# Performance work log

Measured on AMD Instinct MI355X. Metric: run time of the kernel, lower is better.

## Reference

```python
import jax, jax.numpy as jnp
import numpy as np

DIM = 1024
EXP = 4           # expansion_factor
NUM_EXPERTS = 4
BATCH, SEQ = 4, 4096


def setup_inputs() -> dict:
    key = jax.random.key(0)
    ks = jax.random.split(key, 6)
    x = jax.random.normal(ks[0], (BATCH, SEQ, DIM), dtype=jnp.float32)
    token_mask = jax.random.randint(ks[1], (BATCH, SEQ), 0, NUM_EXPERTS, dtype=jnp.int32)
    hid = DIM * EXP
    s1 = 1.0 / np.sqrt(DIM)
    s2 = 1.0 / np.sqrt(hid)
    # nn.Linear layout: weight [out_features, in_features]
    w1 = jax.random.uniform(ks[2], (hid, DIM), minval=-s1, maxval=s1, dtype=jnp.float32)
    b1 = jax.random.uniform(ks[3], (hid,), minval=-s1, maxval=s1, dtype=jnp.float32)
    w2 = jax.random.uniform(ks[4], (DIM, hid), minval=-s2, maxval=s2, dtype=jnp.float32)
    b2 = jax.random.uniform(ks[5], (DIM,), minval=-s2, maxval=s2, dtype=jnp.float32)
    return {"x": x, "w1": w1, "b1": b1, "w2": w2, "b2": b2, "token_mask": token_mask}


def _nested_ffn(x, w1, b1, w2, b2, token_mask):
    dim = x.shape[-1]            # in_features of proj1
    out_dim = w2.shape[0]        # out_features of proj2 (== dim)
    # Expert m uses the first D_m = width >> (E-1-m) features (matryoshka nesting).
    # Expand (proj1): truncating input features to D_m and doing a full GEMM is
    # exactly equivalent to zeroing features >= D_m, so we mask then do one GEMM.
    d_in = dim >> (NUM_EXPERTS - 1 - token_mask)             # [B,S]
    in_mask = jnp.arange(dim) < d_in[..., None]              # [B,S,dim]
    h = jnp.einsum('bsd,fd->bsf', jnp.where(in_mask, x, jnp.zeros((), x.dtype)), w1) + b1
    h = jax.nn.gelu(h, approximate=False)                    # torch nn.GELU() default = erf
    # Contract (proj2): expert m produces only the first D_m outputs (incl. bias),
    # padded with zeros -> compute full GEMM then mask outputs.
    d_out = out_dim >> (NUM_EXPERTS - 1 - token_mask)        # [B,S]
    out_mask = jnp.arange(out_dim) < d_out[..., None]        # [B,S,out_dim]
    y = jnp.einsum('bsf,df->bsd', h, w2) + b2
    return jnp.where(out_mask, y, jnp.zeros((), y.dtype))


def reference(x, w1, b1, w2, b2, token_mask):
    return _nested_ffn(x, w1, b1, w2, b2, token_mask)
```

## Files before the change

kernel.cpp:

```cpp
#include <hip/hip_runtime.h>
#include <hip/hip_bf16.h>


typedef __bf16 bf16x8 __attribute__((ext_vector_type(8)));
typedef float f32x4 __attribute__((ext_vector_type(4)));

#define M_TOK   16384
#define DIM     1024
#define HID     4096

#define META_T     31
#define META_BLK   64
#define META_MAP   256
#define META_RT    2560

__device__ inline unsigned int pk_bf16(float a, float b) {
  unsigned int r;
  asm("v_cvt_pk_bf16_f32 %0, %1, %2" : "=v"(r) : "v"(a), "v"(b));
  return r;
}

__device__ inline float gelu_f(float v) {
  float v2 = v * v;
  float w = v * fmaf(0.10294324f, v2, 2.30220830f);
  float e = __builtin_amdgcn_exp2f(-w);
  return v * __builtin_amdgcn_rcpf(1.0f + e);
}

__device__ inline void async_copy16(const void* g, void* s) {
  __builtin_amdgcn_global_load_lds(
      (const __attribute__((address_space(1))) unsigned int*)g,
      (__attribute__((address_space(3))) unsigned int*)s,
      16, 0, 0);
}

template<int ROWS, int LDK>
__device__ inline void stage_tile(const unsigned short* __restrict__ g,
                                  int row0, int k0, char* lds) {
  const char* gbase = (const char*)g;
  int tid = threadIdx.x;
#pragma unroll
  for (int i = 0; i < ROWS / 32; ++i) {
    int q = i * 256 + tid;
    int r = q >> 3;
    int c = q & 7;
    int gc = c ^ (r & 7);
    const void* gp = gbase + ((size_t)(row0 + r) * LDK + (size_t)k0 + gc * 8) * 2;
    async_copy16(gp, lds + (size_t)q * 16);
  }
}

__global__ __launch_bounds__(1024) void sort_kernel(const int* __restrict__ tm,
                                                    int* __restrict__ meta) {
  __shared__ int cnt[1024][5];
  __shared__ int sbase[5];
  __shared__ int cb[128];
  __shared__ int pfx[129];
  int tid = threadIdx.x;

  int c0 = 0, c1 = 0, c2 = 0, c3 = 0;
  unsigned int epack = 0;
  int4 tv[4];
#pragma unroll
  for (int j = 0; j < 4; ++j)
    tv[j] = *(const int4*)(tm + tid * 16 + j * 4);
#pragma unroll
  for (int j = 0; j < 4; ++j) {
    int e;
    e = tv[j].x; epack |= (unsigned)e << (2 * (4 * j + 0)); c0 += (e == 0); c1 += (e == 1); c2 += (e == 2); c3 += (e == 3);
    e = tv[j].y; epack |= (unsigned)e << (2 * (4 * j + 1)); c0 += (e == 0); c1 += (e == 1); c2 += (e == 2); c3 += (e == 3);
    e = tv[j].z; epack |= (unsigned)e << (2 * (4 * j + 2)); c0 += (e == 0); c1 += (e == 1); c2 += (e == 2); c3 += (e == 3);
    e = tv[j].w; epack |= (unsigned)e << (2 * (4 * j + 3)); c0 += (e == 0); c1 += (e == 1); c2 += (e == 2); c3 += (e == 3);
  }
  cnt[tid][0] = c0; cnt[tid][1] = c1; cnt[tid][2] = c2; cnt[tid][3] = c3;
  __syncthreads();
  for (int s = 1; s < 1024; s <<= 1) {
    int v0 = 0, v1 = 0, v2 = 0, v3 = 0;
    if (tid >= s) {
      v0 = cnt[tid - s][0]; v1 = cnt[tid - s][1];
      v2 = cnt[tid - s][2]; v3 = cnt[tid - s][3];
    }
    __syncthreads();
    cnt[tid][0] += v0; cnt[tid][1] += v1; cnt[tid][2] += v2; cnt[tid][3] += v3;
    __syncthreads();
  }
  if (tid == 0) {
    int b = 0;
#pragma unroll
    for (int e = 0; e < 4; ++e) { sbase[e] = b; b += cnt[1023][e]; }
    sbase[4] = b;
  }
  __syncthreads();
  int off0 = sbase[0] + cnt[tid][0] - c0;
  int off1 = sbase[1] + cnt[tid][1] - c1;
  int off2 = sbase[2] + cnt[tid][2] - c2;
  int off3 = sbase[3] + cnt[tid][3] - c3;
  int* rowtok = meta + META_RT;
#pragma unroll
  for (int j = 0; j < 16; ++j) {
    int e = (epack >> (2 * j)) & 3;
    int t = tid * 16 + j;
    int pos = (e == 0) ? off0++ : (e == 1) ? off1++ : (e == 2) ? off2++ : off3++;
    rowtok[pos] = t | (e << 14);
  }
  if (tid < 128) {
    int last = tid * 128 + 127;
    int e = (last >= sbase[1]) + (last >= sbase[2]) + (last >= sbase[3]);
    cb[tid] = 1 << e;
    meta[META_BLK + tid] = 128 << e;
  }
  __syncthreads();
  if (tid == 0) {
    int acc = 0;
    for (int j = 0; j < 128; ++j) { pfx[j] = acc; acc += cb[j]; }
    pfx[128] = acc;
    meta[META_T] = acc;
  }
  __syncthreads();
  if (tid < 128) {
    int n = cb[tid];
    int p = pfx[tid];
    int* map = meta + META_MAP;
    for (int c = 0; c < n; ++c) map[p + c] = tid * 8 + c;
    int zp = pfx[128] + 8 * tid - pfx[tid];
    for (int c = n; c < 8; ++c) map[zp + (c - n)] = tid * 8 + c;
  }
}

__global__ void prep_kernel(const float* __restrict__ x,
                            const float* __restrict__ w1,
                            const float* __restrict__ w2,
                            const int* __restrict__ meta,
                            unsigned short* __restrict__ xb,
                            unsigned short* __restrict__ w1b,
                            unsigned short* __restrict__ w2b) {
  int b = blockIdx.x;
  int tid = threadIdx.x;
  if (b < M_TOK) {
    int mt = meta[META_RT + b];
    int t = mt & 0x3FFF;
    int din = 128 << (mt >> 14);
    int kb = meta[META_BLK + (b >> 7)];
    int d = tid * 4;
    if (d < kb) {
      uint2 o; o.x = 0; o.y = 0;
      if (d < din) {
        float4 v = *(const float4*)(x + (size_t)t * DIM + d);
        o.x = pk_bf16(v.x, v.y);
        o.y = pk_bf16(v.z, v.w);
      }
      *(uint2*)(xb + (size_t)b * DIM + d) = o;
    }
  } else {
    size_t i = (size_t)(b - M_TOK) * 1024 + tid * 4;
    const float* src;
    unsigned short* dst;
    if (i < (size_t)HID * DIM) { src = w1; dst = w1b; }
    else { src = w2 - (size_t)HID * DIM; dst = w2b - (size_t)HID * DIM; }
    float4 v = *(const float4*)(src + i);
    uint2 o;
    o.x = pk_bf16(v.x, v.y);
    o.y = pk_bf16(v.z, v.w);
    *(uint2*)(dst + i) = o;
  }
}

__global__ __launch_bounds__(256) void gemm1_kernel(
    const unsigned short* __restrict__ A,
    const unsigned short* __restrict__ B,
    const float* __restrict__ bias,
    const int* __restrict__ meta,
    unsigned short* __restrict__ H)
{
  constexpr int K = DIM, N = HID;
  __shared__ char smem[32768];
  char* As = smem;
  char* Bs = smem + 16384;
  int tid = threadIdx.x;
  int lane = tid & 63, quad = lane >> 4, l15 = lane & 15;
  int wave = tid >> 6, wm = wave & 1, wn = wave >> 1;
  int rowblk = 127 - (blockIdx.x >> 5);
  int row0 = rowblk * 128, col0 = (blockIdx.x & 31) * 128;
  int kmax = meta[META_BLK + rowblk];

  int chb = (quad ^ (l15 & 7)) << 4;

  f32x4 acc[4][4] = {};

  for (int k0 = 0; k0 < kmax; k0 += 64) {
    __syncthreads();
    stage_tile<128, K>(A, row0, k0, As);
    stage_tile<128, K>(B, col0, k0, Bs);
    __syncthreads();
#pragma unroll
    for (int kk = 0; kk < 2; ++kk) {
      int xo = chb ^ (kk << 6);
      bf16x8 af[4], bg[4];
#pragma unroll
      for (int mt = 0; mt < 4; ++mt)
        af[mt] = *(const bf16x8*)(As + (wm * 64 + mt * 16 + l15) * 128 + xo);
#pragma unroll
      for (int nt = 0; nt < 4; ++nt)
        bg[nt] = *(const bf16x8*)(Bs + (wn * 64 + nt * 16 + l15) * 128 + xo);
#pragma unroll
      for (int mt = 0; mt < 4; ++mt)
#pragma unroll
        for (int nt = 0; nt < 4; ++nt)
          acc[mt][nt] = __builtin_amdgcn_mfma_f32_16x16x32_bf16(
              bg[nt], af[mt], acc[mt][nt], 0, 0, 0);
    }
  }

  int t_base = row0 + wm * 64;
  int f_base = col0 + wn * 64;
#pragma unroll
  for (int nt = 0; nt < 4; ++nt) {
    int f0 = f_base + nt * 16 + quad * 4;
    float4 bv = *(const float4*)(bias + f0);
#pragma unroll
    for (int mt = 0; mt < 4; ++mt) {
      int t = t_base + mt * 16 + l15;
      float v0 = gelu_f(acc[mt][nt][0] + bv.x);
      float v1 = gelu_f(acc[mt][nt][1] + bv.y);
      float v2 = gelu_f(acc[mt][nt][2] + bv.z);
      float v3 = gelu_f(acc[mt][nt][3] + bv.w);
      uint2 p;
      p.x = pk_bf16(v0, v1);
      p.y = pk_bf16(v2, v3);
      *(uint2*)(H + (size_t)t * N + f0) = p;
    }
  }
}

__global__ __launch_bounds__(256) void gemm2_kernel(
    const unsigned short* __restrict__ A,
    const unsigned short* __restrict__ B,
    const float* __restrict__ bias,
    const int* __restrict__ meta,
    float* __restrict__ out)
{
  constexpr int K = HID, N = DIM;
  int T = meta[META_T];
  int b = blockIdx.x;
  int mp = meta[META_MAP + b];
  int row0 = (mp >> 3) * 128, col0 = (mp & 7) * 128;
  const int* rowtok = meta + META_RT;
  int tid = threadIdx.x;

  if (b >= T) {
    float4 z = make_float4(0.f, 0.f, 0.f, 0.f);
#pragma unroll
    for (int i = 0; i < 16; ++i) {
      int idx = i * 256 + tid;
      int r = idx >> 5;
      int col = (idx & 31) * 4;
      int t = rowtok[row0 + r] & 0x3FFF;
      *(float4*)(out + (size_t)t * N + col0 + col) = z;
    }
    return;
  }

  __shared__ char smem[32768];
  char* As = smem;
  char* Bs = smem + 16384;
  int lane = tid & 63, quad = lane >> 4, l15 = lane & 15;
  int wave = tid >> 6, wm = wave & 1, wn = wave >> 1;
  int chb = (quad ^ (l15 & 7)) << 4;

  f32x4 acc[4][4] = {};

  for (int k0 = 0; k0 < K; k0 += 64) {
    __syncthreads();
    stage_tile<128, K>(A, row0, k0, As);
    stage_tile<128, K>(B, col0, k0, Bs);
    __syncthreads();
#pragma unroll
    for (int kk = 0; kk < 2; ++kk) {
      int xo = chb ^ (kk << 6);
      bf16x8 af[4], bg[4];
#pragma unroll
      for (int mt = 0; mt < 4; ++mt)
        af[mt] = *(const bf16x8*)(As + (wm * 64 + mt * 16 + l15) * 128 + xo);
#pragma unroll
      for (int nt = 0; nt < 4; ++nt)
        bg[nt] = *(const bf16x8*)(Bs + (wn * 64 + nt * 16 + l15) * 128 + xo);
#pragma unroll
      for (int mt = 0; mt < 4; ++mt)
#pragma unroll
        for (int nt = 0; nt < 4; ++nt)
          acc[mt][nt] = __builtin_amdgcn_mfma_f32_16x16x32_bf16(
              bg[nt], af[mt], acc[mt][nt], 0, 0, 0);
    }
  }

  int p_base = row0 + wm * 64;
  int d_base = col0 + wn * 64;
  float4 bv[4];
#pragma unroll
  for (int nt = 0; nt < 4; ++nt)
    bv[nt] = *(const float4*)(bias + d_base + nt * 16 + quad * 4);
#pragma unroll
  for (int mt = 0; mt < 4; ++mt) {
    int m2 = rowtok[p_base + mt * 16 + l15];
    int t = m2 & 0x3FFF;
    int dout = 128 << (m2 >> 14);
#pragma unroll
    for (int nt = 0; nt < 4; ++nt) {
      int d0 = d_base + nt * 16 + quad * 4;
      bool ok = d0 < dout;
      float4 o;
      o.x = ok ? acc[mt][nt][0] + bv[nt].x : 0.0f;
      o.y = ok ? acc[mt][nt][1] + bv[nt].y : 0.0f;
      o.z = ok ? acc[mt][nt][2] + bv[nt].z : 0.0f;
      o.w = ok ? acc[mt][nt][3] + bv[nt].w : 0.0f;
      *(float4*)(out + (size_t)t * N + d0) = o;
    }
  }
}

extern "C" void kernel_launch(void* const* d_in, const int* in_sizes, int n_in,
                              void* d_out, int out_size, void* d_ws, size_t ws_size,
                              hipStream_t stream) {
  const float* x  = (const float*)d_in[0];
  const float* w1 = (const float*)d_in[1];
  const float* b1 = (const float*)d_in[2];
  const float* w2 = (const float*)d_in[3];
  const float* b2 = (const float*)d_in[4];
  const int*   tm = (const int*)d_in[5];
  float* out = (float*)d_out;

  char* ws = (char*)d_ws;
  int* meta = (int*)ws;
  unsigned short* xb  = (unsigned short*)(ws + 131072);
  unsigned short* w1b = (unsigned short*)(ws + 33685504);
  unsigned short* w2b = (unsigned short*)(ws + 42074112);
  unsigned short* hb  = (unsigned short*)(ws + 50462720);

  sort_kernel<<<1, 1024, 0, stream>>>(tm, meta);
  prep_kernel<<<M_TOK + 8192, 256, 0, stream>>>(x, w1, w2, meta, xb, w1b, w2b);
  gemm1_kernel<<<4096, 256, 0, stream>>>(xb, w1b, b1, meta, hb);
  gemm2_kernel<<<1024, 256, 0, stream>>>(hb, w2b, b2, meta, out);
}
```

Baseline: 348.1 us.

## Overlap token sort with weight conversion and use wave-shuffle scans

Moves the single-block token sort into block 0 of a new kernel whose other 2048 blocks convert w1/w2 to bf16, so the serial sort runs alongside the weight conversion instead of before it. The sort replaces the 10-step LDS Hillis-Steele scan with wave-level shuffle scans on packed 16-bit counts, and writes the row map to LDS before coalesced global stores. The x gather/convert becomes its own kernel that runs after the sort. The cost is an extra kernel launch, and block 0 of the merged kernel carries the full sort, which may leave it as a straggler.

```diff
diff --git a/kernel.cpp b/kernel.cpp
--- a/kernel.cpp
+++ b/kernel.cpp
@@ -50,109 +50,16 @@
   }
 }
 
-__global__ __launch_bounds__(1024) void sort_kernel(const int* __restrict__ tm,
-                                                    int* __restrict__ meta) {
-  __shared__ int cnt[1024][5];
-  __shared__ int sbase[5];
-  __shared__ int cb[128];
-  __shared__ int pfx[129];
-  int tid = threadIdx.x;
-
-  int c0 = 0, c1 = 0, c2 = 0, c3 = 0;
-  unsigned int epack = 0;
-  int4 tv[4];
-#pragma unroll
-  for (int j = 0; j < 4; ++j)
-    tv[j] = *(const int4*)(tm + tid * 16 + j * 4);
-#pragma unroll
-  for (int j = 0; j < 4; ++j) {
-    int e;
-    e = tv[j].x; epack |= (unsigned)e << (2 * (4 * j + 0)); c0 += (e == 0); c1 += (e == 1); c2 += (e == 2); c3 += (e == 3);
-    e = tv[j].y; epack |= (unsigned)e << (2 * (4 * j + 1)); c0 += (e == 0); c1 += (e == 1); c2 += (e == 2); c3 += (e == 3);
-    e = tv[j].z; epack |= (unsigned)e << (2 * (4 * j + 2)); c0 += (e == 0); c1 += (e == 1); c2 += (e == 2); c3 += (e == 3);
-    e = tv[j].w; epack |= (unsigned)e << (2 * (4 * j + 3)); c0 += (e == 0); c1 += (e == 1); c2 += (e == 2); c3 += (e == 3);
-  }
-  cnt[tid][0] = c0; cnt[tid][1] = c1; cnt[tid][2] = c2; cnt[tid][3] = c3;
-  __syncthreads();
-  for (int s = 1; s < 1024; s <<= 1) {
-    int v0 = 0, v1 = 0, v2 = 0, v3 = 0;
-    if (tid >= s) {
-      v0 = cnt[tid - s][0]; v1 = cnt[tid - s][1];
-      v2 = cnt[tid - s][2]; v3 = cnt[tid - s][3];
-    }
-    __syncthreads();
-    cnt[tid][0] += v0; cnt[tid][1] += v1; cnt[tid][2] += v2; cnt[tid][3] += v3;
-    __syncthreads();
-  }
-  if (tid == 0) {
-    int b = 0;
-#pragma unroll
-    for (int e = 0; e < 4; ++e) { sbase[e] = b; b += cnt[1023][e]; }
-    sbase[4] = b;
-  }
-  __syncthreads();
-  int off0 = sbase[0] + cnt[tid][0] - c0;
-  int off1 = sbase[1] + cnt[tid][1] - c1;
-  int off2 = sbase[2] + cnt[tid][2] - c2;
-  int off3 = sbase[3] + cnt[tid][3] - c3;
-  int* rowtok = meta + META_RT;
-#pragma unroll
-  for (int j = 0; j < 16; ++j) {
-    int e = (epack >> (2 * j)) & 3;
-    int t = tid * 16 + j;
-    int pos = (e == 0) ? off0++ : (e == 1) ? off1++ : (e == 2) ? off2++ : off3++;
-    rowtok[pos] = t | (e << 14);
-  }
-  if (tid < 128) {
-    int last = tid * 128 + 127;
-    int e = (last >= sbase[1]) + (last >= sbase[2]) + (last >= sbase[3]);
-    cb[tid] = 1 << e;
-    meta[META_BLK + tid] = 128 << e;
-  }
-  __syncthreads();
-  if (tid == 0) {
-    int acc = 0;
-    for (int j = 0; j < 128; ++j) { pfx[j] = acc; acc += cb[j]; }
-    pfx[128] = acc;
-    meta[META_T] = acc;
-  }
-  __syncthreads();
-  if (tid < 128) {
-    int n = cb[tid];
-    int p = pfx[tid];
-    int* map = meta + META_MAP;
-    for (int c = 0; c < n; ++c) map[p + c] = tid * 8 + c;
-    int zp = pfx[128] + 8 * tid - pfx[tid];
-    for (int c = n; c < 8; ++c) map[zp + (c - n)] = tid * 8 + c;
-  }
-}
-
-__global__ void prep_kernel(const float* __restrict__ x,
-                            const float* __restrict__ w1,
-                            const float* __restrict__ w2,
-                            const int* __restrict__ meta,
-                            unsigned short* __restrict__ xb,
-                            unsigned short* __restrict__ w1b,
-                            unsigned short* __restrict__ w2b) {
-  int b = blockIdx.x;
-  int tid = threadIdx.x;
-  if (b < M_TOK) {
-    int mt = meta[META_RT + b];
-    int t = mt & 0x3FFF;
-    int din = 128 << (mt >> 14);
-    int kb = meta[META_BLK + (b >> 7)];
-    int d = tid * 4;
-    if (d < kb) {
-      uint2 o; o.x = 0; o.y = 0;
-      if (d < din) {
-        float4 v = *(const float4*)(x + (size_t)t * DIM + d);
-        o.x = pk_bf16(v.x, v.y);
-        o.y = pk_bf16(v.z, v.w);
-      }
-      *(uint2*)(xb + (size_t)b * DIM + d) = o;
-    }
-  } else {
-    size_t i = (size_t)(b - M_TOK) * 1024 + tid * 4;
+__global__ __launch_bounds__(1024) void sortw_kernel(
+    const int* __restrict__ tm,
+    const float* __restrict__ w1,
+    const float* __restrict__ w2,
+    int* __restrict__ meta,
+    unsigned short* __restrict__ w1b,
+    unsigned short* __restrict__ w2b) {
+  int tid = threadIdx.x;
+  if (blockIdx.x != 0) {
+    size_t i = (size_t)(blockIdx.x - 1) * 4096 + tid * 4;
     const float* src;
     unsigned short* dst;
     if (i < (size_t)HID * DIM) { src = w1; dst = w1b; }
@@ -162,6 +69,123 @@
     o.x = pk_bf16(v.x, v.y);
     o.y = pk_bf16(v.z, v.w);
     *(uint2*)(dst + i) = o;
+    return;
+  }
+
+  __shared__ unsigned short rt[16384];
+  __shared__ unsigned int w01[16], w23[16];
+  __shared__ int sbase[4];
+  __shared__ int cb[128];
+  __shared__ int pfx[129];
+  int lane = tid & 63, wv = tid >> 6;
+
+  int c0 = 0, c1 = 0, c2 = 0, c3 = 0;
+  unsigned int epack = 0;
+  int4 tv[4];
+#pragma unroll
+  for (int j = 0; j < 4; ++j)
+    tv[j] = *(const int4*)(tm + tid * 16 + j * 4);
+#pragma unroll
+  for (int j = 0; j < 4; ++j) {
+    int e;
+    e = tv[j].x; epack |= (unsigned)e << (2 * (4 * j + 0)); c0 += (e == 0); c1 += (e == 1); c2 += (e == 2); c3 += (e == 3);
+    e = tv[j].y; epack |= (unsigned)e << (2 * (4 * j + 1)); c0 += (e == 0); c1 += (e == 1); c2 += (e == 2); c3 += (e == 3);
+    e = tv[j].z; epack |= (unsigned)e << (2 * (4 * j + 2)); c0 += (e == 0); c1 += (e == 1); c2 += (e == 2); c3 += (e == 3);
+    e = tv[j].w; epack |= (unsigned)e << (2 * (4 * j + 3)); c0 += (e == 0); c1 += (e == 1); c2 += (e == 2); c3 += (e == 3);
+  }
+  unsigned int p01 = (unsigned)c0 | ((unsigned)c1 << 16);
+  unsigned int p23 = (unsigned)c2 | ((unsigned)c3 << 16);
+  unsigned int i01 = p01, i23 = p23;
+#pragma unroll
+  for (int s = 1; s < 64; s <<= 1) {
+    unsigned int t0 = __shfl_up(i01, s, 64);
+    unsigned int t1 = __shfl_up(i23, s, 64);
+    if (lane >= s) { i01 += t0; i23 += t1; }
+  }
+  if (lane == 63) { w01[wv] = i01; w23[wv] = i23; }
+  unsigned int e01 = i01 - p01, e23 = i23 - p23;
+  __syncthreads();
+  if (tid < 16) {
+    unsigned int a = w01[tid], b = w23[tid];
+    unsigned int ia = a, ib = b;
+#pragma unroll
+    for (int s = 1; s < 16; s <<= 1) {
+      unsigned int t0 = __shfl_up(ia, s, 64);
+      unsigned int t1 = __shfl_up(ib, s, 64);
+      if (tid >= s) { ia += t0; ib += t1; }
+    }
+    w01[tid] = ia - a;
+    w23[tid] = ib - b;
+    if (tid == 15) {
+      int t0 = (int)(ia & 0xFFFF), t1 = (int)(ia >> 16), t2 = (int)(ib & 0xFFFF);
+      sbase[0] = 0; sbase[1] = t0; sbase[2] = t0 + t1; sbase[3] = t0 + t1 + t2;
+    }
+  }
+  __syncthreads();
+  int off0 = sbase[0] + (int)((w01[wv] & 0xFFFF) + (e01 & 0xFFFF));
+  int off1 = sbase[1] + (int)((w01[wv] >> 16) + (e01 >> 16));
+  int off2 = sbase[2] + (int)((w23[wv] & 0xFFFF) + (e23 & 0xFFFF));
+  int off3 = sbase[3] + (int)((w23[wv] >> 16) + (e23 >> 16));
+#pragma unroll
+  for (int j = 0; j < 16; ++j) {
+    int e = (epack >> (2 * j)) & 3;
+    int t = tid * 16 + j;
+    int pos = (e == 0) ? off0++ : (e == 1) ? off1++ : (e == 2) ? off2++ : off3++;
+    rt[pos] = (unsigned short)(t | (e << 14));
+  }
+  __syncthreads();
+
+  if (tid < 64) {
+    int s0 = tid * 2, s1 = s0 + 1;
+    int l0 = s0 * 128 + 127, l1 = s1 * 128 + 127;
+    int e0 = (l0 >= sbase[1]) + (l0 >= sbase[2]) + (l0 >= sbase[3]);
+    int e1 = (l1 >= sbase[1]) + (l1 >= sbase[2]) + (l1 >= sbase[3]);
+    int v0 = 1 << e0, v1 = 1 << e1, pair = v0 + v1;
+    meta[META_BLK + s0] = 128 << e0;
+    meta[META_BLK + s1] = 128 << e1;
+    cb[s0] = v0; cb[s1] = v1;
+    int inc = pair;
+#pragma unroll
+    for (int s = 1; s < 64; s <<= 1) {
+      int t = __shfl_up(inc, s, 64);
+      if (tid >= s) inc += t;
+    }
+    int excl = inc - pair;
+    pfx[s0] = excl; pfx[s1] = excl + v0;
+    if (tid == 63) { pfx[128] = inc; meta[META_T] = inc; }
+  }
+  __syncthreads();
+  if (tid < 128) {
+    int n = cb[tid], p = pfx[tid];
+    int* map = meta + META_MAP;
+    for (int c = 0; c < n; ++c) map[p + c] = tid * 8 + c;
+    int zp = pfx[128] + 8 * tid - pfx[tid];
+    for (int c = n; c < 8; ++c) map[zp + (c - n)] = tid * 8 + c;
+  }
+  int* rowtok = meta + META_RT;
+#pragma unroll
+  for (int j = 0; j < 16; ++j)
+    rowtok[j * 1024 + tid] = (int)rt[j * 1024 + tid];
+}
+
+__global__ void prepx_kernel(const float* __restrict__ x,
+                             const int* __restrict__ meta,
+                             unsigned short* __restrict__ xb) {
+  int b = blockIdx.x;
+  int tid = threadIdx.x;
+  int mt = meta[META_RT + b];
+  int t = mt & 0x3FFF;
+  int din = 128 << (mt >> 14);
+  int kb = meta[META_BLK + (b >> 7)];
+  int d = tid * 4;
+  if (d < kb) {
+    uint2 o; o.x = 0; o.y = 0;
+    if (d < din) {
+      float4 v = *(const float4*)(x + (size_t)t * DIM + d);
+      o.x = pk_bf16(v.x, v.y);
+      o.y = pk_bf16(v.z, v.w);
+    }
+    *(uint2*)(xb + (size_t)b * DIM + d) = o;
   }
 }
 
@@ -336,8 +360,8 @@
   unsigned short* w2b = (unsigned short*)(ws + 42074112);
   unsigned short* hb  = (unsigned short*)(ws + 50462720);
 
-  sort_kernel<<<1, 1024, 0, stream>>>(tm, meta);
-  prep_kernel<<<M_TOK + 8192, 256, 0, stream>>>(x, w1, w2, meta, xb, w1b, w2b);
+  sortw_kernel<<<2049, 1024, 0, stream>>>(tm, w1, w2, meta, w1b, w2b);
+  prepx_kernel<<<M_TOK, 256, 0, stream>>>(x, meta, xb);
   gemm1_kernel<<<4096, 256, 0, stream>>>(xb, w1b, b1, meta, hb);
   gemm2_kernel<<<1024, 256, 0, stream>>>(hb, w2b, b2, meta, out);
 }
```

Measured after the change: 328.1 us. 1.06x faster.
